# Kernel optimization log

Hardware: AMD Instinct MI355X
Metric: run time of the kernel (lower is better)

## Reference

```python
import jax, jax.numpy as jnp
import numpy as np

N = 96                       # max_num_nodes == input_dim
LATENT = 256
OUT_DIM = N * (N + 1) // 2   # 4656
MPM_ITERS = 50


def setup_inputs() -> dict:
    key = jax.random.key(0)
    ks = jax.random.split(key, 8)
    s = 0.05
    return {
        "input_features": jax.random.normal(ks[0], (1, N, N), jnp.float32),
        "adj": jax.random.uniform(ks[1], (1, N, N), jnp.float32),
        "eps": jax.random.normal(ks[2], (1, LATENT), jnp.float32),
        "We11": jax.random.normal(ks[3], (N * N, LATENT), jnp.float32) * s,
        "be11": jnp.zeros((LATENT,), jnp.float32),
        "We12": jax.random.normal(ks[4], (N * N, LATENT), jnp.float32) * s,
        "be12": jnp.zeros((LATENT,), jnp.float32),
        "Wd1": jax.random.normal(ks[5], (LATENT, LATENT), jnp.float32) * s,
        "bd1": jnp.zeros((LATENT,), jnp.float32),
        "Wd2": jax.random.normal(ks[6], (LATENT, OUT_DIM), jnp.float32) * s,
        "bd2": jnp.zeros((OUT_DIM,), jnp.float32),
    }


def _bce(inp, tgt):
    # torch F.binary_cross_entropy(input=inp, target=tgt) with log clamp -100
    li = jnp.clip(jnp.log(inp), -100.0)
    l1 = jnp.clip(jnp.log1p(-inp), -100.0)
    return -jnp.mean(tgt * li + (1.0 - tgt) * l1)


def reference(input_features, adj, eps, We11, be11, We12, be12, Wd1, bd1, Wd2, bd2):
    # ---- MLP_VAE_plain ----
    h = input_features.reshape(-1, N * N)              # [1, N*N]
    z_mu = h @ We11 + be11
    z_ls = h @ We12 + be12
    z = eps * jnp.exp(0.5 * z_ls) + z_mu
    y = jax.nn.relu(z @ Wd1 + bd1) @ Wd2 + bd2         # [1, OUT_DIM]
    out = jax.nn.sigmoid(y)

    # ---- recover recon adjacency from triu vector (detached in original) ----
    iu, ju = jnp.triu_indices(N)
    up = jnp.zeros((N, N), jnp.float32).at[iu, ju].set(out[0])
    adj_rec = up + up.T - jnp.diag(jnp.diag(up))

    adj0 = adj[0]
    feat = jnp.sum(adj0, axis=1)                       # degree features
    feat_r = jnp.sum(adj_rec, axis=1)

    # ---- edge similarity tensor S[i,j,a,b] (vectorized O(N^4)) ----
    d = jnp.diag(adj0)
    dr = jnp.diag(adj_rec)
    A = adj0 * d[:, None] * d[None, :]                 # adj[i,j]*adj[i,i]*adj[j,j]
    B = adj_rec * dr[:, None] * dr[None, :]
    off = 1.0 - jnp.eye(N, dtype=jnp.float32)
    S = (A * off)[:, :, None, None] * (B * off)[None, None, :, :]  # i!=j, a!=b
    sim = 1.0 / (jnp.abs(feat[:, None] - feat_r[None, :]) + 1.0)   # deg_feature_similarity
    Sd = d[:, None] * dr[None, :] * sim                # S[i,i,a,a]
    r = jnp.arange(N)
    S = S.at[r[:, None], r[:, None], r[None, :], r[None, :]].set(Sd)

    # ---- max-pool matching (mpm), 50 iterations ----
    x0 = jnp.full((N, N), 1.0 / N, jnp.float32)

    def step(x, _):
        pooled = jnp.max(S * x[None, :, None, :], axis=3)          # [i,j,a]
        x_new = x * Sd + jnp.einsum('ija,ij->ia', pooled, off)     # sum over j != i
        return x_new / jnp.linalg.norm(x_new), None

    assignment, _ = jax.lax.scan(step, x0, None, length=MPM_ITERS)
    # (original then calls scipy Hungarian and only prints; result is unused in loss)

    # ---- loss ----
    adj_vec = adj0[iu, ju]                             # detached in original
    recon_loss = _bce(adj_vec, out[0])
    kl = -0.5 * jnp.sum(1.0 + z_ls - z_mu ** 2 - jnp.exp(z_ls)) / (N * N)
    loss = recon_loss + kl
    return loss, assignment
```

## Files before the change

kernel.cpp:

```cpp
#include <hip/hip_runtime.h>
#include <math.h>

typedef unsigned long long ull;

#define N      96
#define NN     9216
#define LAT    256
#define ODIM   4656
#define CH     128
#define RPC    72
#define ITERS  50
#define CB     12
#define CT     768
#define CPB    8
#define WPT    6

#define SENT_F   -1.0f
#define SENT_U   0xBF800000u
#define SENTPAIR 0xBF800000BF800000ULL

#define WS_PART  0
#define WS_OUTS  65536
#define WS_KL    70192
#define WS_BCE   70193
#define WS_NSLOT 70208
#define WS_XBUF  70976

__device__ __forceinline__ int tri(int i, int j) {
    return i * N - i * (i - 1) / 2 + (j - i);
}

__device__ __forceinline__ int tri_row(int o) {
    int i = (int)floorf((193.0f - sqrtf((float)(37249 - 8 * o))) * 0.5f);
    i = max(0, min(95, i));
    while ((i + 1) * N - (i + 1) * i / 2 <= o) ++i;
    while (i * N - i * (i - 1) / 2 > o) --i;
    return i;
}

__global__ __launch_bounds__(256) void kA_gemv(const float* __restrict__ h,
                                               const float* __restrict__ W1,
                                               const float* __restrict__ W2,
                                               float* __restrict__ ws) {
    __shared__ float hs[RPC];
    int t = threadIdx.x, c = blockIdx.x;
    if (c == 0) {
        if (t < 2) ws[WS_KL + t] = 0.f;
        for (int z = t; z < 4 * CB * 16; z += 256) ws[WS_NSLOT + z] = SENT_F;
        for (int z = t; z < 3 * NN; z += 256) ws[WS_XBUF + NN + z] = SENT_F;
    }
    int k0 = c * RPC;
    if (t < RPC) hs[t] = h[k0 + t];
    __syncthreads();
    float a1 = 0.f, a2 = 0.f;
    #pragma unroll 4
    for (int kk = 0; kk < RPC; ++kk) {
        float hv = hs[kk];
        a1 = fmaf(hv, W1[(k0 + kk) * LAT + t], a1);
        a2 = fmaf(hv, W2[(k0 + kk) * LAT + t], a2);
    }
    ws[WS_PART + c * LAT + t]        = a1;
    ws[WS_PART + (CH + c) * LAT + t] = a2;
}

__global__ __launch_bounds__(256) void kB_dec(const float* __restrict__ eps,
                                              const float* __restrict__ be11,
                                              const float* __restrict__ be12,
                                              const float* __restrict__ Wd1,
                                              const float* __restrict__ bd1,
                                              const float* __restrict__ Wd2,
                                              const float* __restrict__ bd2,
                                              const float* __restrict__ adj,
                                              float* __restrict__ ws) {
    __shared__ float zi[LAT];
    __shared__ float hid[LAT];
    __shared__ float red[256];
    int t = threadIdx.x;
    const float* p = ws + WS_PART;
    float mu = 0.f, ls = 0.f;
    #pragma unroll 8
    for (int c = 0; c < CH; ++c) {
        mu += p[c * LAT + t];
        ls += p[(CH + c) * LAT + t];
    }
    mu += be11[t];
    ls += be12[t];
    zi[t] = eps[t] * expf(0.5f * ls) + mu;
    red[t] = 1.0f + ls - mu * mu - expf(ls);
    __syncthreads();
    for (int s = 128; s > 0; s >>= 1) {
        if (t < s) red[t] += red[t + s];
        __syncthreads();
    }
    if (blockIdx.x == 0 && t == 0) ws[WS_KL] = -0.5f * red[0] / 9216.0f;
    __syncthreads();
    float acc = 0.f;
    #pragma unroll 8
    for (int k = 0; k < LAT; ++k) acc = fmaf(zi[k], Wd1[k * LAT + t], acc);
    hid[t] = fmaxf(acc + bd1[t], 0.f);
    __syncthreads();
    int o = blockIdx.x * 256 + t;
    float term = 0.f;
    if (o < ODIM) {
        float a2 = 0.f;
        #pragma unroll 8
        for (int k = 0; k < LAT; ++k) a2 = fmaf(hid[k], Wd2[k * ODIM + o], a2);
        float y = a2 + bd2[o];
        float s = 1.0f / (1.0f + expf(-y));
        ws[WS_OUTS + o] = s;
        int i = tri_row(o);
        int j = i + (o - (i * N - i * (i - 1) / 2));
        float inp = adj[i * N + j];
        float li = fmaxf(logf(inp), -100.0f);
        float l1 = fmaxf(log1pf(-inp), -100.0f);
        term = s * li + (1.0f - s) * l1;
    }
    red[t] = term;
    __syncthreads();
    for (int s = 128; s > 0; s >>= 1) {
        if (t < s) red[t] += red[t + s];
        __syncthreads();
    }
    if (t == 0) atomicAdd(ws + WS_BCE, red[0]);
}

__global__ __launch_bounds__(CT, 3) void kC_mpm(const float* __restrict__ adj,
                                                float* __restrict__ ws,
                                                float* __restrict__ out) {
    __shared__ float xnT[N][97];
    __shared__ float Brow[CPB][N];
    __shared__ float Scol[CPB][N];
    __shared__ float Mv[CPB][N];
    __shared__ float ds[N], drs[N], ft[N];
    __shared__ float ftr_sh[CPB];
    __shared__ float wred[CT / 64];
    __shared__ float s_inv;

    int t = threadIdx.x, bid = blockIdx.x;
    int jj = t % N, al = t / N;
    int a  = bid * CPB + al;

    const float* outs = ws + WS_OUTS;
    float* xbuf  = ws + WS_XBUF;
    float* nslot = ws + WS_NSLOT;

    if (t < N) {
        ds[t]  = adj[t * N + t];
        drs[t] = outs[tri(t, t)];
        const float4* ar = (const float4*)(adj + t * N);
        float s1 = 0.f;
        #pragma unroll
        for (int q = 0; q < N / 4; ++q) {
            float4 v = ar[q];
            s1 += v.x + v.y + v.z + v.w;
        }
        ft[t] = s1;
    }
    __syncthreads();
    {
        int lo = min(a, jj), hi = max(a, jj);
        Mv[al][jj] = outs[tri(lo, hi)];
    }
    __syncthreads();
    if (t < CPB) {
        float s2 = 0.f;
        for (int b = 0; b < N; ++b) s2 += Mv[t][b];
        ftr_sh[t] = s2;
    }
    __syncthreads();
    Brow[al][jj] = (jj == a) ? 0.f : (Mv[al][jj] * drs[a]) * drs[jj];
    Scol[al][jj] = (ds[jj] * drs[a]) * (1.0f / (fabsf(ft[jj] - ftr_sh[al]) + 1.0f));

    float arow[N];
    {
        const float* arp = adj + jj * N;
        float di = ds[jj];
        #pragma unroll
        for (int j = 0; j < N; ++j)
            arow[j] = (j == jj) ? 0.f : (arp[j] * di) * ds[j];
    }
    __syncthreads();

    float acc = 0.f;
    for (int s = 0; s < ITERS; ++s) {
        if (s == 0) {
            const float v0 = (float)(1.0 / 96.0);
            for (int f = t; f < NN; f += CT) xnT[f / N][f % N] = v0;
            if (t == 0) s_inv = 1.0f;
        } else {
            const ull* src = (const ull*)(xbuf + (s & 3) * NN);
            ull v[WPT];
            bool ok = false;
            while (!ok) {
                ok = true;
                #pragma unroll
                for (int k = 0; k < WPT; ++k)
                    v[k] = __hip_atomic_load(&src[k * CT + t], __ATOMIC_RELAXED,
                                             __HIP_MEMORY_SCOPE_AGENT);
                #pragma unroll
                for (int k = 0; k < WPT; ++k) ok &= (v[k] != SENTPAIR);
                if (!ok) __builtin_amdgcn_s_sleep(1);
            }
            #pragma unroll
            for (int k = 0; k < WPT; ++k) {
                int e = (k * CT + t) * 2;
                int ac = e / N, i = e % N;
                xnT[ac][i]     = __uint_as_float((unsigned)v[k]);
                xnT[ac][i + 1] = __uint_as_float((unsigned)(v[k] >> 32));
            }
            if (t < 64) {
                float pv = 0.f;
                bool done = (t >= CB);
                const unsigned* np = (const unsigned*)(nslot + (s & 3) * CB * 16);
                while (!__all(done)) {
                    if (!done) {
                        unsigned u = __hip_atomic_load(&np[t * 16], __ATOMIC_RELAXED,
                                                       __HIP_MEMORY_SCOPE_AGENT);
                        if (u != SENT_U) { pv = __uint_as_float(u); done = true; }
                    }
                    __builtin_amdgcn_s_sleep(1);
                }
                #pragma unroll
                for (int off = 8; off > 0; off >>= 1) pv += __shfl_xor(pv, off, 16);
                if (t == 0) s_inv = 1.0f / sqrtf(pv);
            }
        }
        __syncthreads();

        float m = 0.f;
        #pragma unroll
        for (int b = 0; b < N; ++b)
            m = fmaxf(m, Brow[al][b] * xnT[b][jj]);
        __syncthreads();
        Mv[al][jj] = m;
        __syncthreads();

        float r = xnT[a][jj] * Scol[al][jj];
        #pragma unroll
        for (int j = 0; j < N; ++j)
            r = fmaf(arow[j], Mv[al][j], r);
        acc = r * s_inv;

        float nx = __shfl_down(acc, 1);
        if (s < ITERS - 1 && (t & 1) == 0) {
            ull pv = (ull)__float_as_uint(acc) | ((ull)__float_as_uint(nx) << 32);
            __hip_atomic_store((ull*)(xbuf + ((s + 1) & 3) * NN) + ((a * N + jj) >> 1),
                               pv, __ATOMIC_RELAXED, __HIP_MEMORY_SCOPE_AGENT);
        }

        float ss = acc * acc;
        #pragma unroll
        for (int off = 32; off > 0; off >>= 1) ss += __shfl_xor(ss, off);
        if ((t & 63) == 0) wred[t >> 6] = ss;
        __syncthreads();
        if (t == 0) {
            float sum = 0.f;
            #pragma unroll
            for (int w = 0; w < CT / 64; ++w) sum += wred[w];
            __hip_atomic_store((unsigned*)(nslot + ((s + 1) & 3) * CB * 16 + bid * 16),
                               __float_as_uint(sum), __ATOMIC_RELAXED,
                               __HIP_MEMORY_SCOPE_AGENT);
        }

        if (s < ITERS - 3 && (t & 1) == 0) {
            __hip_atomic_store((ull*)(xbuf + ((s + 3) & 3) * NN) + ((a * N + jj) >> 1),
                               SENTPAIR, __ATOMIC_RELAXED, __HIP_MEMORY_SCOPE_AGENT);
        }
        if (s < ITERS - 2 && t == 0) {
            __hip_atomic_store((unsigned*)(nslot + ((s + 3) & 3) * CB * 16 + bid * 16),
                               SENT_U, __ATOMIC_RELAXED, __HIP_MEMORY_SCOPE_AGENT);
        }
        __syncthreads();
    }

    if (t < 64) {
        float pv = 0.f;
        bool done = (t >= CB);
        const unsigned* np = (const unsigned*)(nslot + (ITERS & 3) * CB * 16);
        while (!__all(done)) {
            if (!done) {
                unsigned u = __hip_atomic_load(&np[t * 16], __ATOMIC_RELAXED,
                                               __HIP_MEMORY_SCOPE_AGENT);
                if (u != SENT_U) { pv = __uint_as_float(u); done = true; }
            }
            __builtin_amdgcn_s_sleep(1);
        }
        #pragma unroll
        for (int off = 8; off > 0; off >>= 1) pv += __shfl_xor(pv, off, 16);
        if (t == 0) s_inv = 1.0f / sqrtf(pv);
    }
    __syncthreads();
    out[1 + jj * N + a] = acc * s_inv;
    if (bid == 0 && t == 0)
        out[0] = -(ws[WS_BCE] / 4656.0f) + ws[WS_KL];
}

extern "C" void kernel_launch(void* const* d_in, const int* in_sizes, int n_in,
                              void* d_out, int out_size, void* d_ws, size_t ws_size,
                              hipStream_t stream) {
    const float* inf  = (const float*)d_in[0];
    const float* adj  = (const float*)d_in[1];
    const float* eps  = (const float*)d_in[2];
    const float* We11 = (const float*)d_in[3];
    const float* be11 = (const float*)d_in[4];
    const float* We12 = (const float*)d_in[5];
    const float* be12 = (const float*)d_in[6];
    const float* Wd1  = (const float*)d_in[7];
    const float* bd1  = (const float*)d_in[8];
    const float* Wd2  = (const float*)d_in[9];
    const float* bd2  = (const float*)d_in[10];
    float* ws  = (float*)d_ws;
    float* out = (float*)d_out;

    kA_gemv<<<CH, 256, 0, stream>>>(inf, We11, We12, ws);
    kB_dec <<<19, 256, 0, stream>>>(eps, be11, be12, Wd1, bd1, Wd2, bd2, adj, ws);
    kC_mpm <<<CB, CT, 0, stream>>>(adj, ws, out);
}
```

Before: 379.7 us.

## Transpose MPM exchange buffer layout, vectorize LDS reads, and trim per-iteration barriers

Global exchange buffer of x now stores x transposed (jj*N+a), so each block writes scattered scalars and readers pull contiguous 6-ull chunks into a row-major padded LDS array via float4 stores. Both inner loops (max-pool and weighted sum) now use float4 LDS reads, and the norm-slot wait is moved after the max-pool computation to overlap with it. Two block barriers per iteration are removed, and sentinel reset of the buffer is spread across all GEMV blocks. Scattered 4-byte atomic stores replace paired 8-byte stores, which may raise global traffic, and arow is pinned in registers via asm.

```diff
diff --git a/kernel.cpp b/kernel.cpp
--- a/kernel.cpp
+++ b/kernel.cpp
@@ -13,7 +13,6 @@
 #define CB     12
 #define CT     768
 #define CPB    8
-#define WPT    6
 
 #define SENT_F   -1.0f
 #define SENT_U   0xBF800000u
@@ -47,8 +46,8 @@
     if (c == 0) {
         if (t < 2) ws[WS_KL + t] = 0.f;
         for (int z = t; z < 4 * CB * 16; z += 256) ws[WS_NSLOT + z] = SENT_F;
-        for (int z = t; z < 3 * NN; z += 256) ws[WS_XBUF + NN + z] = SENT_F;
-    }
+    }
+    for (int z = c * 256 + t; z < 4 * NN; z += CH * 256) ws[WS_XBUF + z] = SENT_F;
     int k0 = c * RPC;
     if (t < RPC) hs[t] = h[k0 + t];
     __syncthreads();
@@ -127,10 +126,10 @@
 __global__ __launch_bounds__(CT, 3) void kC_mpm(const float* __restrict__ adj,
                                                 float* __restrict__ ws,
                                                 float* __restrict__ out) {
-    __shared__ float xnT[N][97];
-    __shared__ float Brow[CPB][N];
-    __shared__ float Scol[CPB][N];
-    __shared__ float Mv[CPB][N];
+    __shared__ __align__(16) float xn[N][100];
+    __shared__ __align__(16) float Brow[CPB][N];
+    __shared__ __align__(16) float Scol[CPB][N];
+    __shared__ __align__(16) float Mv[CPB][N];
     __shared__ float ds[N], drs[N], ft[N];
     __shared__ float ftr_sh[CPB];
     __shared__ float wred[CT / 64];
@@ -139,6 +138,7 @@
     int t = threadIdx.x, bid = blockIdx.x;
     int jj = t % N, al = t / N;
     int a  = bid * CPB + al;
+    int si = t >> 3, sc = t & 7;
 
     const float* outs = ws + WS_OUTS;
     float* xbuf  = ws + WS_XBUF;
@@ -179,79 +179,95 @@
         for (int j = 0; j < N; ++j)
             arow[j] = (j == jj) ? 0.f : (arp[j] * di) * ds[j];
     }
+    #pragma unroll
+    for (int j = 0; j < N; ++j) asm volatile("" : "+v"(arow[j]));
     __syncthreads();
 
     float acc = 0.f;
     for (int s = 0; s < ITERS; ++s) {
         if (s == 0) {
             const float v0 = (float)(1.0 / 96.0);
-            for (int f = t; f < NN; f += CT) xnT[f / N][f % N] = v0;
+            for (int f = t; f < NN; f += CT) xn[f / N][f % N] = v0;
             if (t == 0) s_inv = 1.0f;
         } else {
-            const ull* src = (const ull*)(xbuf + (s & 3) * NN);
-            ull v[WPT];
+            const ull* src = (const ull*)(xbuf + (s & 3) * NN) + (si * 48 + sc * 6);
+            union { ull u[6]; float4 q[3]; } U;
             bool ok = false;
             while (!ok) {
                 ok = true;
                 #pragma unroll
-                for (int k = 0; k < WPT; ++k)
-                    v[k] = __hip_atomic_load(&src[k * CT + t], __ATOMIC_RELAXED,
-                                             __HIP_MEMORY_SCOPE_AGENT);
+                for (int k = 0; k < 6; ++k)
+                    U.u[k] = __hip_atomic_load(&src[k], __ATOMIC_RELAXED,
+                                               __HIP_MEMORY_SCOPE_AGENT);
                 #pragma unroll
-                for (int k = 0; k < WPT; ++k) ok &= (v[k] != SENTPAIR);
+                for (int k = 0; k < 6; ++k) {
+                    ok &= ((unsigned)U.u[k] != SENT_U);
+                    ok &= ((unsigned)(U.u[k] >> 32) != SENT_U);
+                }
                 if (!ok) __builtin_amdgcn_s_sleep(1);
             }
+            float4* dst = (float4*)&xn[si][sc * 12];
+            dst[0] = U.q[0]; dst[1] = U.q[1]; dst[2] = U.q[2];
+        }
+        __syncthreads();
+
+        float m = 0.f;
+        #pragma unroll
+        for (int q = 0; q < N / 4; ++q) {
+            float4 xv = *(const float4*)&xn[jj][q * 4];
+            float4 bw = *(const float4*)&Brow[al][q * 4];
+            m = fmaxf(m, bw.x * xv.x);
+            m = fmaxf(m, bw.y * xv.y);
+            m = fmaxf(m, bw.z * xv.z);
+            m = fmaxf(m, bw.w * xv.w);
+        }
+        Mv[al][jj] = m;
+
+        if (s > 0 && t < 64) {
+            float pv = 0.f;
+            bool done = (t >= CB);
+            const unsigned* np = (const unsigned*)(nslot + (s & 3) * CB * 16);
+            while (!__all(done)) {
+                if (!done) {
+                    unsigned u = __hip_atomic_load(&np[t * 16], __ATOMIC_RELAXED,
+                                                   __HIP_MEMORY_SCOPE_AGENT);
+                    if (u != SENT_U) { pv = __uint_as_float(u); done = true; }
+                }
+                __builtin_amdgcn_s_sleep(1);
+            }
             #pragma unroll
-            for (int k = 0; k < WPT; ++k) {
-                int e = (k * CT + t) * 2;
-                int ac = e / N, i = e % N;
-                xnT[ac][i]     = __uint_as_float((unsigned)v[k]);
-                xnT[ac][i + 1] = __uint_as_float((unsigned)(v[k] >> 32));
-            }
-            if (t < 64) {
-                float pv = 0.f;
-                bool done = (t >= CB);
-                const unsigned* np = (const unsigned*)(nslot + (s & 3) * CB * 16);
-                while (!__all(done)) {
-                    if (!done) {
-                        unsigned u = __hip_atomic_load(&np[t * 16], __ATOMIC_RELAXED,
-                                                       __HIP_MEMORY_SCOPE_AGENT);
-                        if (u != SENT_U) { pv = __uint_as_float(u); done = true; }
-                    }
-                    __builtin_amdgcn_s_sleep(1);
-                }
-                #pragma unroll
-                for (int off = 8; off > 0; off >>= 1) pv += __shfl_xor(pv, off, 16);
-                if (t == 0) s_inv = 1.0f / sqrtf(pv);
-            }
-        }
-        __syncthreads();
-
-        float m = 0.f;
-        #pragma unroll
-        for (int b = 0; b < N; ++b)
-            m = fmaxf(m, Brow[al][b] * xnT[b][jj]);
-        __syncthreads();
-        Mv[al][jj] = m;
-        __syncthreads();
-
-        float r = xnT[a][jj] * Scol[al][jj];
-        #pragma unroll
-        for (int j = 0; j < N; ++j)
-            r = fmaf(arow[j], Mv[al][j], r);
+            for (int off = 8; off > 0; off >>= 1) pv += __shfl_xor(pv, off, 16);
+            if (t == 0) s_inv = 1.0f / sqrtf(pv);
+        }
+        __syncthreads();
+
+        float r = xn[jj][a] * Scol[al][jj];
+        #pragma unroll
+        for (int q = 0; q < N / 4; ++q) {
+            float4 mv = *(const float4*)&Mv[al][q * 4];
+            r = fmaf(arow[q * 4 + 0], mv.x, r);
+            r = fmaf(arow[q * 4 + 1], mv.y, r);
+            r = fmaf(arow[q * 4 + 2], mv.z, r);
+            r = fmaf(arow[q * 4 + 3], mv.w, r);
+        }
         acc = r * s_inv;
 
-        float nx = __shfl_down(acc, 1);
-        if (s < ITERS - 1 && (t & 1) == 0) {
-            ull pv = (ull)__float_as_uint(acc) | ((ull)__float_as_uint(nx) << 32);
-            __hip_atomic_store((ull*)(xbuf + ((s + 1) & 3) * NN) + ((a * N + jj) >> 1),
-                               pv, __ATOMIC_RELAXED, __HIP_MEMORY_SCOPE_AGENT);
-        }
-
-        float ss = acc * acc;
-        #pragma unroll
-        for (int off = 32; off > 0; off >>= 1) ss += __shfl_xor(ss, off);
-        if ((t & 63) == 0) wred[t >> 6] = ss;
+        if (s < ITERS - 1)
+            __hip_atomic_store((unsigned*)(xbuf + ((s + 1) & 3) * NN) + (jj * N + a),
+                               __float_as_uint(acc), __ATOMIC_RELAXED,
+                               __HIP_MEMORY_SCOPE_AGENT);
+        if (s < ITERS - 3) {
+            ull* rb = (ull*)(xbuf + ((s + 3) & 3) * NN) + (si * 48 + sc * 6);
+            #pragma unroll
+            for (int k = 0; k < 6; ++k)
+                __hip_atomic_store(&rb[k], SENTPAIR, __ATOMIC_RELAXED,
+                                   __HIP_MEMORY_SCOPE_AGENT);
+        }
+
+        float ssq = acc * acc;
+        #pragma unroll
+        for (int off = 32; off > 0; off >>= 1) ssq += __shfl_xor(ssq, off);
+        if ((t & 63) == 0) wred[t >> 6] = ssq;
         __syncthreads();
         if (t == 0) {
             float sum = 0.f;
@@ -260,17 +276,11 @@
             __hip_atomic_store((unsigned*)(nslot + ((s + 1) & 3) * CB * 16 + bid * 16),
                                __float_as_uint(sum), __ATOMIC_RELAXED,
                                __HIP_MEMORY_SCOPE_AGENT);
-        }
-
-        if (s < ITERS - 3 && (t & 1) == 0) {
-            __hip_atomic_store((ull*)(xbuf + ((s + 3) & 3) * NN) + ((a * N + jj) >> 1),
-                               SENTPAIR, __ATOMIC_RELAXED, __HIP_MEMORY_SCOPE_AGENT);
-        }
-        if (s < ITERS - 2 && t == 0) {
-            __hip_atomic_store((unsigned*)(nslot + ((s + 3) & 3) * CB * 16 + bid * 16),
-                               SENT_U, __ATOMIC_RELAXED, __HIP_MEMORY_SCOPE_AGENT);
-        }
-        __syncthreads();
+            if (s < ITERS - 2)
+                __hip_atomic_store((unsigned*)(nslot + ((s + 3) & 3) * CB * 16 + bid * 16),
+                                   SENT_U, __ATOMIC_RELAXED,
+                                   __HIP_MEMORY_SCOPE_AGENT);
+        }
     }
 
     if (t < 64) {
```

Result: slower. 663.7 us (+74.8%).
